# Performance work log

Hardware: AMD Instinct MI355X
Metric: run time of the kernel (lower is better)

## Reference

```python
import jax, jax.numpy as jnp
import numpy as np

D_MODEL = 1024

def setup_inputs() -> dict:
    key = jax.random.key(0)
    ks = jax.random.split(key, 7)
    s = 1.0 / np.sqrt(D_MODEL)
    x = jax.random.normal(ks[0], (4, 2048, D_MODEL), dtype=jnp.float32)
    wq_w = jax.random.uniform(ks[1], (D_MODEL, D_MODEL), jnp.float32, -s, s)
    wq_b = jax.random.uniform(ks[2], (D_MODEL,), jnp.float32, -s, s)
    wk_w = jax.random.uniform(ks[3], (D_MODEL, D_MODEL), jnp.float32, -s, s)
    wk_b = jax.random.uniform(ks[4], (D_MODEL,), jnp.float32, -s, s)
    wv_w = jax.random.uniform(ks[5], (D_MODEL, D_MODEL), jnp.float32, -s, s)
    wv_b = jax.random.uniform(ks[6], (D_MODEL,), jnp.float32, -s, s)
    return {"x": x, "wq_w": wq_w, "wq_b": wq_b, "wk_w": wk_w, "wk_b": wk_b, "wv_w": wv_w, "wv_b": wv_b}

def reference(x, wq_w, wq_b, wk_w, wk_b, wv_w, wv_b):
    # Linear: x @ W^T + b (torch nn.Linear convention)
    q = jnp.einsum('bsd,ed->bse', x, wq_w) + wq_b
    k = jnp.einsum('bsd,ed->bse', x, wk_w) + wk_b
    v = jnp.einsum('bsd,ed->bse', x, wv_w) + wv_b
    scale = 1.0 / jnp.sqrt(jnp.asarray(k.shape[-1], dtype=q.dtype))
    logits = jnp.einsum('bqd,bkd->bqk', q, k) * scale  # [B, S, S]
    attn = jax.nn.softmax(logits, axis=-1)
    out = jnp.einsum('bqk,bkd->bqd', attn, v)
    return (attn, out)
```

## Files before the change

### kernel.cpp

```cpp
#include <hip/hip_runtime.h>

typedef unsigned short u16;
typedef u16 u16x4 __attribute__((ext_vector_type(4)));
typedef u16 u16x8 __attribute__((ext_vector_type(8)));
typedef __bf16 bf16x8 __attribute__((ext_vector_type(8)));
typedef float f32x4 __attribute__((ext_vector_type(4)));

static __device__ __forceinline__ u16 f2bf(float f) {
  unsigned u = __builtin_bit_cast(unsigned, f);
  u += 0x7fffu + ((u >> 16) & 1u);
  return (u16)(u >> 16);
}
static __device__ __forceinline__ float bf2f(u16 h) {
  return __builtin_bit_cast(float, ((unsigned)h) << 16);
}

static __device__ __forceinline__ void gload_lds16(const u16* g, u16* l) {
  u16* gn = const_cast<u16*>(g);
  __builtin_amdgcn_global_load_lds(
      (__attribute__((address_space(1))) unsigned int*)gn,
      (__attribute__((address_space(3))) unsigned int*)l,
      16, 0, 0);
}

__global__ __launch_bounds__(256)
void cvt_f32_bf16(const float* __restrict__ in, u16* __restrict__ out) {
  const int i = blockIdx.x * 256 + threadIdx.x;
  float4 f = ((const float4*)in)[i];
  u16x4 o = { f2bf(f.x), f2bf(f.y), f2bf(f.z), f2bf(f.w) };
  ((u16x4*)out)[i] = o;
}

template<int MODE>
__global__ __launch_bounds__(256)
void gemm_bt(const u16* __restrict__ Ain, const u16* __restrict__ Bin,
             void* __restrict__ Cv, const float* __restrict__ bias,
             int lda, int ldb, int ldc, int K, float alpha,
             unsigned long long sA, unsigned long long sB, unsigned long long sC)
{
  constexpr int BM = 128, BN = 128, BK = 32;
  __shared__ alignas(16) u16 As[BM * BK];
  __shared__ alignas(16) u16 Bs[BN * BK];

  const u16* A = Ain + blockIdx.z * sA;
  const u16* B = Bin + blockIdx.z * sB;

  const int tid  = threadIdx.x;
  const int wave = tid >> 6;
  const int lane = tid & 63;
  const int quad = lane >> 4;
  const int l16  = lane & 15;
  const int wr   = wave >> 1;
  const int wc   = wave & 1;

  const int m0 = blockIdx.y * BM;
  const int n0 = blockIdx.x * BN;

  const u16* Ag = A + (size_t)(m0 + wave * 32 + (lane >> 2)) * lda + (lane & 3) * 8;
  const u16* Bg = B + (size_t)(n0 + wave * 32 + (lane >> 2)) * ldb + (lane & 3) * 8;
  u16* As0 = &As[(wave * 32 + 0)  * BK];
  u16* As1 = &As[(wave * 32 + 16) * BK];
  u16* Bs0 = &Bs[(wave * 32 + 0)  * BK];
  u16* Bs1 = &Bs[(wave * 32 + 16) * BK];

  f32x4 acc[4][4];
  #pragma unroll
  for (int i = 0; i < 4; ++i)
    #pragma unroll
    for (int j = 0; j < 4; ++j)
      acc[i][j] = (f32x4){0.f, 0.f, 0.f, 0.f};

  for (int k0 = 0; k0 < K; k0 += BK) {
    gload_lds16(Ag + k0,                    As0);
    gload_lds16(Ag + (size_t)16 * lda + k0, As1);
    gload_lds16(Bg + k0,                    Bs0);
    gload_lds16(Bg + (size_t)16 * ldb + k0, Bs1);
    __syncthreads();

    bf16x8 af[4], bfr[4];
    #pragma unroll
    for (int mi = 0; mi < 4; ++mi)
      af[mi] = *(const bf16x8*)&As[(wr * 64 + mi * 16 + l16) * BK + quad * 8];
    #pragma unroll
    for (int ni = 0; ni < 4; ++ni)
      bfr[ni] = *(const bf16x8*)&Bs[(wc * 64 + ni * 16 + l16) * BK + quad * 8];

    #pragma unroll
    for (int mi = 0; mi < 4; ++mi)
      #pragma unroll
      for (int ni = 0; ni < 4; ++ni)
        acc[mi][ni] = __builtin_amdgcn_mfma_f32_16x16x32_bf16(af[mi], bfr[ni], acc[mi][ni], 0, 0, 0);

    __syncthreads();
  }

  const int mbase = m0 + wr * 64 + quad * 4;
  const int nbase = n0 + wc * 64 + l16;

  if constexpr (MODE == 0) {
    u16* Cb = (u16*)Cv;
    #pragma unroll
    for (int ni = 0; ni < 4; ++ni) {
      const int col = nbase + ni * 16;
      const float bv = bias[col];
      #pragma unroll
      for (int mi = 0; mi < 4; ++mi) {
        const size_t base = (size_t)(mbase + mi * 16) * ldc + col;
        #pragma unroll
        for (int r = 0; r < 4; ++r)
          Cb[base + (size_t)r * ldc] = f2bf(acc[mi][ni][r] + bv);
      }
    }
  } else if constexpr (MODE == 1) {
    u16* Cb = (u16*)Cv;
    #pragma unroll
    for (int ni = 0; ni < 4; ++ni) {
      const int col = nbase + ni * 16;
      const float bv = bias[col];
      #pragma unroll
      for (int mi = 0; mi < 4; ++mi) {
        const int row = mbase + mi * 16;
        u16x4 o;
        #pragma unroll
        for (int r = 0; r < 4; ++r) o[r] = f2bf(acc[mi][ni][r] + bv);
        const size_t idx = ((size_t)((row >> 11) * 1024 + col)) * 2048 + (row & 2047);
        *(u16x4*)&Cb[idx] = o;
      }
    }
  } else if constexpr (MODE == 2) {
    u16* Cb = (u16*)Cv + blockIdx.z * sC;
    #pragma unroll
    for (int ni = 0; ni < 4; ++ni) {
      const int col = nbase + ni * 16;
      #pragma unroll
      for (int mi = 0; mi < 4; ++mi) {
        const size_t base = (size_t)(mbase + mi * 16) * ldc + col;
        #pragma unroll
        for (int r = 0; r < 4; ++r)
          Cb[base + (size_t)r * ldc] = f2bf(acc[mi][ni][r] * alpha);
      }
    }
  } else {
    float* Cf = (float*)Cv + blockIdx.z * sC;
    #pragma unroll
    for (int ni = 0; ni < 4; ++ni) {
      const int col = nbase + ni * 16;
      #pragma unroll
      for (int mi = 0; mi < 4; ++mi) {
        const size_t base = (size_t)(mbase + mi * 16) * ldc + col;
        #pragma unroll
        for (int r = 0; r < 4; ++r)
          Cf[base + (size_t)r * ldc] = acc[mi][ni][r];
      }
    }
  }
}

__global__ __launch_bounds__(256)
void softmax_rows(u16* __restrict__ logits, float* __restrict__ attn) {
  const int row = blockIdx.x;
  const int tid = threadIdx.x;
  u16*  lp = logits + (size_t)row * 2048 + tid * 8;
  float* ap = attn  + (size_t)row * 2048 + tid * 8;

  u16x8 raw = *(const u16x8*)lp;
  float v[8];
  #pragma unroll
  for (int j = 0; j < 8; ++j) v[j] = bf2f(raw[j]);

  float mx = v[0];
  #pragma unroll
  for (int j = 1; j < 8; ++j) mx = fmaxf(mx, v[j]);
  #pragma unroll
  for (int o = 32; o > 0; o >>= 1) mx = fmaxf(mx, __shfl_xor(mx, o, 64));

  __shared__ float smax[4], ssum[4];
  const int wv = tid >> 6, ln = tid & 63;
  if (ln == 0) smax[wv] = mx;
  __syncthreads();
  mx = fmaxf(fmaxf(smax[0], smax[1]), fmaxf(smax[2], smax[3]));

  float s = 0.f;
  #pragma unroll
  for (int j = 0; j < 8; ++j) { v[j] = __expf(v[j] - mx); s += v[j]; }
  #pragma unroll
  for (int o = 32; o > 0; o >>= 1) s += __shfl_xor(s, o, 64);
  if (ln == 0) ssum[wv] = s;
  __syncthreads();
  s = (ssum[0] + ssum[1]) + (ssum[2] + ssum[3]);
  const float inv = 1.f / s;

  u16x8 ob;
  #pragma unroll
  for (int j = 0; j < 8; ++j) { v[j] *= inv; ob[j] = f2bf(v[j]); }
  float4* apv = (float4*)ap;
  apv[0] = make_float4(v[0], v[1], v[2], v[3]);
  apv[1] = make_float4(v[4], v[5], v[6], v[7]);
  *(u16x8*)lp = ob;
}

extern "C" void kernel_launch(void* const* d_in, const int* in_sizes, int n_in,
                              void* d_out, int out_size, void* d_ws, size_t ws_size,
                              hipStream_t stream) {
  (void)in_sizes; (void)n_in; (void)out_size; (void)ws_size;
  const float* x    = (const float*)d_in[0];
  const float* wq_w = (const float*)d_in[1];
  const float* wq_b = (const float*)d_in[2];
  const float* wk_w = (const float*)d_in[3];
  const float* wk_b = (const float*)d_in[4];
  const float* wv_w = (const float*)d_in[5];
  const float* wv_b = (const float*)d_in[6];

  float* attn = (float*)d_out;
  float* outp = attn + 16777216ULL;

  u16* xb  = (u16*)d_ws;
  u16* wqb = xb  + 8388608ULL;
  u16* wkb = wqb + 1048576ULL;
  u16* wvb = wkb + 1048576ULL;
  u16* Qb  = wvb + 1048576ULL;
  u16* Kb  = Qb  + 8388608ULL;
  u16* Vt  = Kb  + 8388608ULL;
  u16* Lg  = Vt  + 8388608ULL;

  cvt_f32_bf16<<<8192, 256, 0, stream>>>(x,    xb);
  cvt_f32_bf16<<<1024, 256, 0, stream>>>(wq_w, wqb);
  cvt_f32_bf16<<<1024, 256, 0, stream>>>(wk_w, wkb);
  cvt_f32_bf16<<<1024, 256, 0, stream>>>(wv_w, wvb);

  gemm_bt<0><<<dim3(8, 64, 1), 256, 0, stream>>>(xb, wqb, Qb, wq_b, 1024, 1024, 1024, 1024, 1.f, 0, 0, 0);
  gemm_bt<0><<<dim3(8, 64, 1), 256, 0, stream>>>(xb, wkb, Kb, wk_b, 1024, 1024, 1024, 1024, 1.f, 0, 0, 0);
  gemm_bt<1><<<dim3(8, 64, 1), 256, 0, stream>>>(xb, wvb, Vt, wv_b, 1024, 1024, 0,    1024, 1.f, 0, 0, 0);

  gemm_bt<2><<<dim3(16, 16, 4), 256, 0, stream>>>(Qb, Kb, Lg, nullptr, 1024, 1024, 2048, 1024, 0.03125f,
                                                  2097152ULL, 2097152ULL, 4194304ULL);
  softmax_rows<<<8192, 256, 0, stream>>>(Lg, attn);

  gemm_bt<3><<<dim3(8, 16, 4), 256, 0, stream>>>(Lg, Vt, outp, nullptr, 2048, 2048, 1024, 2048, 1.f,
                                                 4194304ULL, 2097152ULL, 2097152ULL);
}
```

Measured before the change: 374.3 us.

## Fuse QKV projections, deepen K tile, swizzle LDS, and remap blocks for L2 locality

The three weight conversions and three projection GEMMs are merged into one conversion kernel and one GEMM over a concatenated weight matrix, with the epilogue routing each column range to Q, K, or transposed V with its own bias. The GEMM K tile is doubled to 64 with an XOR-swizzled LDS layout, which halves the number of barriers per K and is meant to avoid bank conflicts. Blocks are remapped from a 1D grid with XCD-aware interleaving and grouped tile ordering so that tiles sharing operands run close together in time and reuse L2. Doubling LDS per block may lower occupancy.

```diff
diff --git a/kernel.cpp b/kernel.cpp
--- a/kernel.cpp
+++ b/kernel.cpp
@@ -31,19 +31,45 @@
   ((u16x4*)out)[i] = o;
 }
 
+__global__ __launch_bounds__(256)
+void cvt_w3(const float* __restrict__ a, const float* __restrict__ b,
+            const float* __restrict__ c, u16* __restrict__ out) {
+  const int blk = blockIdx.x;
+  const int w = blk >> 10;
+  const float* src = (w == 0) ? a : (w == 1) ? b : c;
+  const int i = (blk & 1023) * 256 + threadIdx.x;
+  float4 f = ((const float4*)src)[i];
+  u16x4 o = { f2bf(f.x), f2bf(f.y), f2bf(f.z), f2bf(f.w) };
+  ((u16x4*)(out + (size_t)w * 1048576ULL))[i] = o;
+}
+
 template<int MODE>
 __global__ __launch_bounds__(256)
 void gemm_bt(const u16* __restrict__ Ain, const u16* __restrict__ Bin,
-             void* __restrict__ Cv, const float* __restrict__ bias,
+             void* __restrict__ Cv,
+             const float* __restrict__ b0, const float* __restrict__ b1,
+             const float* __restrict__ b2,
              int lda, int ldb, int ldc, int K, float alpha,
-             unsigned long long sA, unsigned long long sB, unsigned long long sC)
+             unsigned long long sA, unsigned long long sB, unsigned long long sC,
+             int nbx, int nby)
 {
-  constexpr int BM = 128, BN = 128, BK = 32;
+  constexpr int BM = 128, BN = 128, BK = 64;
   __shared__ alignas(16) u16 As[BM * BK];
   __shared__ alignas(16) u16 Bs[BN * BK];
 
-  const u16* A = Ain + blockIdx.z * sA;
-  const u16* B = Bin + blockIdx.z * sB;
+  const int nbxy = nbx * nby;
+  const int bid  = blockIdx.x;
+  const int flat = (bid & 7) * ((int)gridDim.x >> 3) + (bid >> 3);
+  const int z    = flat / nbxy;
+  const int rr   = flat - z * nbxy;
+  const int width = nbx << 3;
+  const int gid  = rr / width;
+  const int rw   = rr - gid * width;
+  const int by   = (gid << 3) + (rw & 7);
+  const int bx   = rw >> 3;
+
+  const u16* A = Ain + z * sA;
+  const u16* B = Bin + z * sB;
 
   const int tid  = threadIdx.x;
   const int wave = tid >> 6;
@@ -53,15 +79,15 @@
   const int wr   = wave >> 1;
   const int wc   = wave & 1;
 
-  const int m0 = blockIdx.y * BM;
-  const int n0 = blockIdx.x * BN;
-
-  const u16* Ag = A + (size_t)(m0 + wave * 32 + (lane >> 2)) * lda + (lane & 3) * 8;
-  const u16* Bg = B + (size_t)(n0 + wave * 32 + (lane >> 2)) * ldb + (lane & 3) * 8;
-  u16* As0 = &As[(wave * 32 + 0)  * BK];
-  u16* As1 = &As[(wave * 32 + 16) * BK];
-  u16* Bs0 = &Bs[(wave * 32 + 0)  * BK];
-  u16* Bs1 = &Bs[(wave * 32 + 16) * BK];
+  const int m0 = by * BM;
+  const int n0 = bx * BN;
+
+  const int lr = lane >> 3;
+  const int sc = ((lane & 7) ^ lr) * 8;
+  const u16* Ag = A + (size_t)(m0 + wave * 32 + lr) * lda + sc;
+  const u16* Bg = B + (size_t)(n0 + wave * 32 + lr) * ldb + sc;
+  u16* Asb = &As[(wave * 32) * BK];
+  u16* Bsb = &Bs[(wave * 32) * BK];
 
   f32x4 acc[4][4];
   #pragma unroll
@@ -71,26 +97,35 @@
       acc[i][j] = (f32x4){0.f, 0.f, 0.f, 0.f};
 
   for (int k0 = 0; k0 < K; k0 += BK) {
-    gload_lds16(Ag + k0,                    As0);
-    gload_lds16(Ag + (size_t)16 * lda + k0, As1);
-    gload_lds16(Bg + k0,                    Bs0);
-    gload_lds16(Bg + (size_t)16 * ldb + k0, Bs1);
+    gload_lds16(Ag + k0,                    Asb);
+    gload_lds16(Ag + (size_t) 8 * lda + k0, Asb +  8 * BK);
+    gload_lds16(Ag + (size_t)16 * lda + k0, Asb + 16 * BK);
+    gload_lds16(Ag + (size_t)24 * lda + k0, Asb + 24 * BK);
+    gload_lds16(Bg + k0,                    Bsb);
+    gload_lds16(Bg + (size_t) 8 * ldb + k0, Bsb +  8 * BK);
+    gload_lds16(Bg + (size_t)16 * ldb + k0, Bsb + 16 * BK);
+    gload_lds16(Bg + (size_t)24 * ldb + k0, Bsb + 24 * BK);
     __syncthreads();
 
-    bf16x8 af[4], bfr[4];
-    #pragma unroll
-    for (int mi = 0; mi < 4; ++mi)
-      af[mi] = *(const bf16x8*)&As[(wr * 64 + mi * 16 + l16) * BK + quad * 8];
-    #pragma unroll
-    for (int ni = 0; ni < 4; ++ni)
-      bfr[ni] = *(const bf16x8*)&Bs[(wc * 64 + ni * 16 + l16) * BK + quad * 8];
-
-    #pragma unroll
-    for (int mi = 0; mi < 4; ++mi)
-      #pragma unroll
-      for (int ni = 0; ni < 4; ++ni)
-        acc[mi][ni] = __builtin_amdgcn_mfma_f32_16x16x32_bf16(af[mi], bfr[ni], acc[mi][ni], 0, 0, 0);
-
+    #pragma unroll
+    for (int ks = 0; ks < 2; ++ks) {
+      bf16x8 af[4], bfr[4];
+      #pragma unroll
+      for (int mi = 0; mi < 4; ++mi) {
+        const int row = wr * 64 + mi * 16 + l16;
+        af[mi] = *(const bf16x8*)&As[row * BK + ((((ks << 2) + quad) ^ (l16 & 7)) << 3)];
+      }
+      #pragma unroll
+      for (int ni = 0; ni < 4; ++ni) {
+        const int row = wc * 64 + ni * 16 + l16;
+        bfr[ni] = *(const bf16x8*)&Bs[row * BK + ((((ks << 2) + quad) ^ (l16 & 7)) << 3)];
+      }
+      #pragma unroll
+      for (int mi = 0; mi < 4; ++mi)
+        #pragma unroll
+        for (int ni = 0; ni < 4; ++ni)
+          acc[mi][ni] = __builtin_amdgcn_mfma_f32_16x16x32_bf16(af[mi], bfr[ni], acc[mi][ni], 0, 0, 0);
+    }
     __syncthreads();
   }
 
@@ -98,50 +133,55 @@
   const int nbase = n0 + wc * 64 + l16;
 
   if constexpr (MODE == 0) {
-    u16* Cb = (u16*)Cv;
+    const int g = n0 >> 10;
+    u16* Qb = (u16*)Cv;
+    if (g < 2) {
+      u16* Cb = Qb + (size_t)g * 8388608ULL;
+      const float* bp = (g == 0) ? b0 : b1;
+      #pragma unroll
+      for (int ni = 0; ni < 4; ++ni) {
+        const int col = (nbase + ni * 16) & 1023;
+        const float bv = bp[col];
+        #pragma unroll
+        for (int mi = 0; mi < 4; ++mi) {
+          const size_t base = (size_t)(mbase + mi * 16) * 1024 + col;
+          #pragma unroll
+          for (int r = 0; r < 4; ++r)
+            Cb[base + (size_t)r * 1024] = f2bf(acc[mi][ni][r] + bv);
+        }
+      }
+    } else {
+      u16* Vt = Qb + 16777216ULL;
+      #pragma unroll
+      for (int ni = 0; ni < 4; ++ni) {
+        const int col = (nbase + ni * 16) & 1023;
+        const float bv = b2[col];
+        #pragma unroll
+        for (int mi = 0; mi < 4; ++mi) {
+          const int row = mbase + mi * 16;
+          u16x4 o;
+          #pragma unroll
+          for (int r = 0; r < 4; ++r) o[r] = f2bf(acc[mi][ni][r] + bv);
+          const size_t idx = ((size_t)((row >> 11) * 1024 + col)) * 2048 + (row & 2047);
+          *(u16x4*)&Vt[idx] = o;
+        }
+      }
+    }
+  } else if constexpr (MODE == 2) {
+    u16* Cb = (u16*)Cv + z * sC;
     #pragma unroll
     for (int ni = 0; ni < 4; ++ni) {
       const int col = nbase + ni * 16;
-      const float bv = bias[col];
       #pragma unroll
       for (int mi = 0; mi < 4; ++mi) {
         const size_t base = (size_t)(mbase + mi * 16) * ldc + col;
         #pragma unroll
         for (int r = 0; r < 4; ++r)
-          Cb[base + (size_t)r * ldc] = f2bf(acc[mi][ni][r] + bv);
-      }
-    }
-  } else if constexpr (MODE == 1) {
-    u16* Cb = (u16*)Cv;
-    #pragma unroll
-    for (int ni = 0; ni < 4; ++ni) {
-      const int col = nbase + ni * 16;
-      const float bv = bias[col];
-      #pragma unroll
-      for (int mi = 0; mi < 4; ++mi) {
-        const int row = mbase + mi * 16;
-        u16x4 o;
-        #pragma unroll
-        for (int r = 0; r < 4; ++r) o[r] = f2bf(acc[mi][ni][r] + bv);
-        const size_t idx = ((size_t)((row >> 11) * 1024 + col)) * 2048 + (row & 2047);
-        *(u16x4*)&Cb[idx] = o;
-      }
-    }
-  } else if constexpr (MODE == 2) {
-    u16* Cb = (u16*)Cv + blockIdx.z * sC;
-    #pragma unroll
-    for (int ni = 0; ni < 4; ++ni) {
-      const int col = nbase + ni * 16;
-      #pragma unroll
-      for (int mi = 0; mi < 4; ++mi) {
-        const size_t base = (size_t)(mbase + mi * 16) * ldc + col;
-        #pragma unroll
-        for (int r = 0; r < 4; ++r)
           Cb[base + (size_t)r * ldc] = f2bf(acc[mi][ni][r] * alpha);
       }
     }
   } else {
-    float* Cf = (float*)Cv + blockIdx.z * sC;
+    float* Cf = (float*)Cv + z * sC;
     #pragma unroll
     for (int ni = 0; ni < 4; ++ni) {
       const int col = nbase + ni * 16;
@@ -160,8 +200,8 @@
 void softmax_rows(u16* __restrict__ logits, float* __restrict__ attn) {
   const int row = blockIdx.x;
   const int tid = threadIdx.x;
-  u16*  lp = logits + (size_t)row * 2048 + tid * 8;
-  float* ap = attn  + (size_t)row * 2048 + tid * 8;
+  u16*   lp = logits + (size_t)row * 2048 + tid * 8;
+  float* ap = attn   + (size_t)row * 2048 + tid * 8;
 
   u16x8 raw = *(const u16x8*)lp;
   float v[8];
@@ -214,28 +254,26 @@
   float* attn = (float*)d_out;
   float* outp = attn + 16777216ULL;
 
-  u16* xb  = (u16*)d_ws;
-  u16* wqb = xb  + 8388608ULL;
-  u16* wkb = wqb + 1048576ULL;
-  u16* wvb = wkb + 1048576ULL;
-  u16* Qb  = wvb + 1048576ULL;
-  u16* Kb  = Qb  + 8388608ULL;
-  u16* Vt  = Kb  + 8388608ULL;
-  u16* Lg  = Vt  + 8388608ULL;
-
-  cvt_f32_bf16<<<8192, 256, 0, stream>>>(x,    xb);
-  cvt_f32_bf16<<<1024, 256, 0, stream>>>(wq_w, wqb);
-  cvt_f32_bf16<<<1024, 256, 0, stream>>>(wk_w, wkb);
-  cvt_f32_bf16<<<1024, 256, 0, stream>>>(wv_w, wvb);
-
-  gemm_bt<0><<<dim3(8, 64, 1), 256, 0, stream>>>(xb, wqb, Qb, wq_b, 1024, 1024, 1024, 1024, 1.f, 0, 0, 0);
-  gemm_bt<0><<<dim3(8, 64, 1), 256, 0, stream>>>(xb, wkb, Kb, wk_b, 1024, 1024, 1024, 1024, 1.f, 0, 0, 0);
-  gemm_bt<1><<<dim3(8, 64, 1), 256, 0, stream>>>(xb, wvb, Vt, wv_b, 1024, 1024, 0,    1024, 1.f, 0, 0, 0);
-
-  gemm_bt<2><<<dim3(16, 16, 4), 256, 0, stream>>>(Qb, Kb, Lg, nullptr, 1024, 1024, 2048, 1024, 0.03125f,
-                                                  2097152ULL, 2097152ULL, 4194304ULL);
+  u16* xb   = (u16*)d_ws;
+  u16* wcat = xb   + 8388608ULL;
+  u16* Qb   = wcat + 3145728ULL;
+  u16* Kb   = Qb   + 8388608ULL;
+  u16* Vt   = Kb   + 8388608ULL;
+  u16* Lg   = Vt   + 8388608ULL;
+
+  cvt_f32_bf16<<<8192, 256, 0, stream>>>(x, xb);
+  cvt_w3<<<3072, 256, 0, stream>>>(wq_w, wk_w, wv_w, wcat);
+
+  gemm_bt<0><<<1536, 256, 0, stream>>>(xb, wcat, Qb, wq_b, wk_b, wv_b,
+                                       1024, 1024, 1024, 1024, 1.f, 0, 0, 0, 24, 64);
+
+  gemm_bt<2><<<1024, 256, 0, stream>>>(Qb, Kb, Lg, nullptr, nullptr, nullptr,
+                                       1024, 1024, 2048, 1024, 0.03125f,
+                                       2097152ULL, 2097152ULL, 4194304ULL, 16, 16);
+
   softmax_rows<<<8192, 256, 0, stream>>>(Lg, attn);
 
-  gemm_bt<3><<<dim3(8, 16, 4), 256, 0, stream>>>(Lg, Vt, outp, nullptr, 2048, 2048, 1024, 2048, 1.f,
-                                                 4194304ULL, 2097152ULL, 2097152ULL);
-}
+  gemm_bt<3><<<512, 256, 0, stream>>>(Lg, Vt, outp, nullptr, nullptr, nullptr,
+                                      2048, 2048, 1024, 2048, 1.f,
+                                      4194304ULL, 2097152ULL, 2097152ULL, 8, 16);
+}
```

New measurement: 309.1 us. 1.21x faster.
